# Kernel tuning notes

Measured on AMD Instinct MI355X. Metric: run time of the kernel, lower is better.

Reference implementation:

```python
import jax, jax.numpy as jnp
import numpy as np

QUALITY = 95
X_MIN, X_MAX = 0.0, 1.0

# JPEG Annex K base quantization tables
_LUMA = np.array([
    [16, 11, 10, 16, 24, 40, 51, 61],
    [12, 12, 14, 19, 26, 58, 60, 55],
    [14, 13, 16, 24, 40, 57, 69, 56],
    [14, 17, 22, 29, 51, 87, 80, 62],
    [18, 22, 37, 56, 68, 109, 103, 77],
    [24, 35, 55, 64, 81, 104, 113, 92],
    [49, 64, 78, 87, 103, 121, 120, 101],
    [72, 92, 95, 98, 112, 100, 103, 99]], dtype=np.float32)
_CHROMA = np.array([
    [17, 18, 24, 47, 99, 99, 99, 99],
    [18, 21, 26, 66, 99, 99, 99, 99],
    [24, 26, 56, 99, 99, 99, 99, 99],
    [47, 66, 99, 99, 99, 99, 99, 99],
    [99, 99, 99, 99, 99, 99, 99, 99],
    [99, 99, 99, 99, 99, 99, 99, 99],
    [99, 99, 99, 99, 99, 99, 99, 99],
    [99, 99, 99, 99, 99, 99, 99, 99]], dtype=np.float32)

def _qtable(base, quality):
    # libjpeg quality scaling (quality >= 50 branch)
    scale = 5000.0 / quality if quality < 50 else 200.0 - 2.0 * quality
    return np.clip(np.floor((base * scale + 50.0) / 100.0), 1.0, 255.0).astype(np.float32)

_QL = jnp.asarray(_qtable(_LUMA, QUALITY))
_QC = jnp.asarray(_qtable(_CHROMA, QUALITY))

# Orthonormal 8x8 DCT-II matrix
_k = np.arange(8)
_D = np.sqrt(2.0 / 8.0) * np.cos((2 * _k[None, :] + 1) * _k[:, None] * np.pi / 16.0)
_D[0, :] /= np.sqrt(2.0)
_D = jnp.asarray(_D.astype(np.float32))

def _jpeg_channel(ch, table):
    """8x8 block DCT -> quantize(round) -> dequantize -> IDCT. ch: [B,H,W] level-shifted."""
    B, H, W = ch.shape
    xb = ch.reshape(B, H // 8, 8, W // 8, 8)
    coef = jnp.einsum('ki,bhiwj,lj->bhkwl', _D, xb, _D)
    t = table[None, None, :, None, :]
    deq = jnp.round(coef / t) * t
    rec = jnp.einsum('ki,bhkwl,lj->bhiwj', _D, deq, _D)
    return rec.reshape(B, H, W)

def _jpeg_roundtrip(x255):
    """x255: [B,H,W,3] float values in [0,255]. Simulates JPEG encode+decode (4:2:0)."""
    r, g, b = x255[..., 0], x255[..., 1], x255[..., 2]
    # JFIF RGB -> YCbCr
    y = 0.299 * r + 0.587 * g + 0.114 * b
    cb = -0.168736 * r - 0.331264 * g + 0.5 * b + 128.0
    cr = 0.5 * r - 0.418688 * g - 0.081312 * b + 128.0
    # Luma at full resolution
    y2 = _jpeg_channel(y - 128.0, _QL) + 128.0
    # Chroma: 2x2 average downsample (4:2:0), codec, nearest upsample
    def down(c):
        B, H, W = c.shape
        return c.reshape(B, H // 2, 2, W // 2, 2).mean(axis=(2, 4))
    def up(c):
        return jnp.repeat(jnp.repeat(c, 2, axis=1), 2, axis=2)
    cb2 = up(_jpeg_channel(down(cb) - 128.0, _QC) + 128.0)
    cr2 = up(_jpeg_channel(down(cr) - 128.0, _QC) + 128.0)
    # YCbCr -> RGB
    r2 = y2 + 1.402 * (cr2 - 128.0)
    g2 = y2 - 0.344136 * (cb2 - 128.0) - 0.714136 * (cr2 - 128.0)
    b2 = y2 + 1.772 * (cb2 - 128.0)
    rgb = jnp.stack([r2, g2, b2], axis=-1)
    return jnp.round(jnp.clip(rgb, 0.0, 255.0))  # decoded uint8 values


def setup_inputs() -> dict:
    key = jax.random.key(0)
    x = jax.random.uniform(key, (32, 512, 512, 3), dtype=jnp.float32)
    return {"x": x}


def reference(x):
    # inputs -> uint8 pixel values (tf.cast truncation; values are >= 0)
    x255 = jnp.clip(jnp.floor((x - X_MIN) / ((X_MAX - X_MIN) / 255.0)), 0.0, 255.0)
    dec = _jpeg_roundtrip(x255)
    # back to input range/dtype
    return dec / (255.0 / (X_MAX - X_MIN)) + X_MIN
```

## Files before the change

### kernel.cpp

```cpp
#include <hip/hip_runtime.h>
#include <cstddef>

static constexpr float D8[8][8] = {
  { 0.35355339059327373f, 0.35355339059327373f, 0.35355339059327373f, 0.35355339059327373f,
    0.35355339059327373f, 0.35355339059327373f, 0.35355339059327373f, 0.35355339059327373f},
  { 0.4903926402016152f,  0.4157348061512726f,  0.27778511650980114f, 0.09754516100806417f,
   -0.09754516100806417f,-0.27778511650980114f,-0.4157348061512726f, -0.4903926402016152f},
  { 0.46193976625564337f, 0.19134171618254492f,-0.19134171618254492f,-0.46193976625564337f,
   -0.46193976625564337f,-0.19134171618254492f, 0.19134171618254492f, 0.46193976625564337f},
  { 0.4157348061512726f, -0.09754516100806417f,-0.4903926402016152f, -0.27778511650980114f,
    0.27778511650980114f, 0.4903926402016152f,  0.09754516100806417f,-0.4157348061512726f},
  { 0.35355339059327373f,-0.35355339059327373f,-0.35355339059327373f, 0.35355339059327373f,
    0.35355339059327373f,-0.35355339059327373f,-0.35355339059327373f, 0.35355339059327373f},
  { 0.27778511650980114f,-0.4903926402016152f,  0.09754516100806417f, 0.4157348061512726f,
   -0.4157348061512726f, -0.09754516100806417f, 0.4903926402016152f, -0.27778511650980114f},
  { 0.19134171618254492f,-0.46193976625564337f, 0.46193976625564337f,-0.19134171618254492f,
   -0.19134171618254492f, 0.46193976625564337f,-0.46193976625564337f, 0.19134171618254492f},
  { 0.09754516100806417f,-0.27778511650980114f, 0.4157348061512726f, -0.4903926402016152f,
    0.4903926402016152f, -0.4157348061512726f,  0.27778511650980114f,-0.09754516100806417f},
};

static constexpr float QLt[8][8] = {
  {2,1,1,2,2,4,5,6},
  {1,1,1,2,3,6,6,6},
  {1,1,2,2,4,6,7,6},
  {1,2,2,3,5,9,8,6},
  {2,2,4,6,7,11,10,8},
  {2,4,6,6,8,10,11,9},
  {5,6,8,9,10,12,12,10},
  {7,9,10,10,11,10,10,10},
};
static constexpr float QCt[8][8] = {
  {2,2,2,5,10,10,10,10},
  {2,2,3,7,10,10,10,10},
  {2,3,6,10,10,10,10,10},
  {5,7,10,10,10,10,10,10},
  {10,10,10,10,10,10,10,10},
  {10,10,10,10,10,10,10,10},
  {10,10,10,10,10,10,10,10},
  {10,10,10,10,10,10,10,10},
};

static constexpr float C255  = (float)(1.0/255.0);
static constexpr float RC255 = 1.0f / C255;

__device__ __forceinline__ float exact_div(float x, float c, float r) {
  float q0 = x * r;
  float e  = fmaf(-c, q0, x);
  return fmaf(e, r, q0);
}

__device__ __forceinline__ void dct8(const float x[8], float u[8]) {
  #pragma unroll
  for (int k = 0; k < 8; ++k) {
    float a = D8[k][0] * x[0];
    #pragma unroll
    for (int j = 1; j < 8; ++j) a += D8[k][j] * x[j];
    u[k] = a;
  }
}

__device__ __forceinline__ void idct8(const float x[8], float u[8]) {
  #pragma unroll
  for (int j = 0; j < 8; ++j) {
    float a = x[0] * D8[0][j];
    #pragma unroll
    for (int m = 1; m < 8; ++m) a += x[m] * D8[m][j];
    u[j] = a;
  }
}

__device__ __forceinline__ void xpose_scr(float v[8], int l, float* S) {
  #pragma unroll
  for (int m = 0; m < 8; ++m) S[m*13 + l] = v[m];
  asm volatile("" ::: "memory");
  float u[8];
  #pragma unroll
  for (int m = 0; m < 8; ++m) u[m] = S[l*13 + m];
  asm volatile("" ::: "memory");
  #pragma unroll
  for (int m = 0; m < 8; ++m) v[m] = u[m];
}

__device__ __forceinline__ void quant8(float v[8], const float* QT, const float* RQ) {
  float4 Q0 = *(const float4*)&QT[0];
  float4 Q1 = *(const float4*)&QT[4];
  float4 R0 = *(const float4*)&RQ[0];
  float4 R1 = *(const float4*)&RQ[4];
  float qv[8] = {Q0.x,Q0.y,Q0.z,Q0.w,Q1.x,Q1.y,Q1.z,Q1.w};
  float rv[8] = {R0.x,R0.y,R0.z,R0.w,R1.x,R1.y,R1.z,R1.w};
  #pragma unroll
  for (int m = 0; m < 8; ++m)
    v[m] = rintf(exact_div(v[m], qv[m], rv[m])) * qv[m];
}

__device__ __forceinline__ void jblk8(float v[8], int l, float* S,
                                      const float* QT, const float* RQ) {
  float u[8];
  dct8(v, u);
  xpose_scr(u, l, S);
  dct8(u, v);
  quant8(v, QT, RQ);
  idct8(v, u);
  xpose_scr(u, l, S);
  idct8(u, v);
}

__global__ __launch_bounds__(256) void jpeg_rt(const float* __restrict__ in,
                                               float* __restrict__ out)
{
  __shared__ __align__(16) float Yp[16][132];
  __shared__ __align__(16) float Scr[32][104];
  __shared__ __align__(16) float Cbp[8][68];
  __shared__ __align__(16) float Crp[8][68];
  __shared__ __align__(16) float QTs[2][8][8];
  __shared__ __align__(16) float RQs[2][8][8];

  const int t   = threadIdx.x;
  const int tx  = blockIdx.x;
  const int ty  = blockIdx.y;
  const int img = blockIdx.z;

  const int pr = t >> 5;
  const int pc = t & 31;

  if (t < 128) {
    const int pl = t >> 6, i = (t >> 3) & 7, m = t & 7;
    const float q = pl ? QCt[m][i] : QLt[m][i];
    QTs[pl][i][m] = q;
    RQs[pl][i][m] = 1.0f / q;
  }

  {
    float yv[2][4];
    float cbv[2][4], crv[2][4];
    #pragma unroll
    for (int rr = 0; rr < 2; ++rr) {
      const size_t grow = (size_t)img * 512 + (size_t)(ty*16 + 2*pr + rr);
      const float* rp = in + (grow*512 + (size_t)(tx*128 + 4*pc))*3;
      float4 A = ((const float4*)rp)[0];
      float4 Bq = ((const float4*)rp)[1];
      float4 Cq = ((const float4*)rp)[2];
      float px[12] = {A.x,A.y,A.z,A.w,Bq.x,Bq.y,Bq.z,Bq.w,Cq.x,Cq.y,Cq.z,Cq.w};
      #pragma unroll
      for (int p = 0; p < 4; ++p) {
        float r = floorf(exact_div(px[3*p+0], C255, RC255));
        float g = floorf(exact_div(px[3*p+1], C255, RC255));
        float b = floorf(exact_div(px[3*p+2], C255, RC255));
        float y  =  0.299f*r + 0.587f*g + 0.114f*b;
        float cb = -0.168736f*r - 0.331264f*g + 0.5f*b + 128.0f;
        float cr =  0.5f*r - 0.418688f*g - 0.081312f*b + 128.0f;
        yv[rr][p]  = y - 128.0f;
        cbv[rr][p] = cb;
        crv[rr][p] = cr;
      }
    }
    *(float4*)&Yp[2*pr+0][4*pc] = make_float4(yv[0][0],yv[0][1],yv[0][2],yv[0][3]);
    *(float4*)&Yp[2*pr+1][4*pc] = make_float4(yv[1][0],yv[1][1],yv[1][2],yv[1][3]);
    float cb0 = ((cbv[0][0]+cbv[0][1]) + (cbv[1][0]+cbv[1][1]))*0.25f - 128.0f;
    float cb1 = ((cbv[0][2]+cbv[0][3]) + (cbv[1][2]+cbv[1][3]))*0.25f - 128.0f;
    float cr0 = ((crv[0][0]+crv[0][1]) + (crv[1][0]+crv[1][1]))*0.25f - 128.0f;
    float cr1 = ((crv[0][2]+crv[0][3]) + (crv[1][2]+crv[1][3]))*0.25f - 128.0f;
    *(float2*)&Cbp[pr][2*pc] = make_float2(cb0, cb1);
    *(float2*)&Crp[pr][2*pc] = make_float2(cr0, cr1);
  }
  __syncthreads();

  {
    const int b = t >> 3, l = t & 7;
    const int br = b >> 4, bc = b & 15;
    float* rowp = &Yp[br*8 + l][bc*8];
    float4 L0 = *(const float4*)&rowp[0];
    float4 L1 = *(const float4*)&rowp[4];
    float v[8] = {L0.x, L0.y, L0.z, L0.w, L1.x, L1.y, L1.z, L1.w};
    jblk8(v, l, &Scr[b][0], &QTs[0][l][0], &RQs[0][l][0]);
    *(float4*)&rowp[0] = make_float4(v[0],v[1],v[2],v[3]);
    *(float4*)&rowp[4] = make_float4(v[4],v[5],v[6],v[7]);
  }
  if (t < 128) {
    const int g = t >> 3, l = t & 7;
    float* plane = (g & 8) ? &Crp[0][0] : &Cbp[0][0];
    float* rowp = plane + l*68 + (g & 7)*8;
    float4 L0 = *(const float4*)&rowp[0];
    float4 L1 = *(const float4*)&rowp[4];
    float v[8] = {L0.x, L0.y, L0.z, L0.w, L1.x, L1.y, L1.z, L1.w};
    jblk8(v, l, &Scr[g][0], &QTs[1][l][0], &RQs[1][l][0]);
    *(float4*)&rowp[0] = make_float4(v[0],v[1],v[2],v[3]);
    *(float4*)&rowp[4] = make_float4(v[4],v[5],v[6],v[7]);
  }
  __syncthreads();

  {
    float4 Y0 = *(const float4*)&Yp[2*pr+0][4*pc];
    float4 Y1 = *(const float4*)&Yp[2*pr+1][4*pc];
    float y0[4] = {Y0.x, Y0.y, Y0.z, Y0.w};
    float y1[4] = {Y1.x, Y1.y, Y1.z, Y1.w};
    float2 cbp2 = *(const float2*)&Cbp[pr][2*pc];
    float2 crp2 = *(const float2*)&Crp[pr][2*pc];
    float cbq[2] = {cbp2.x, cbp2.y};
    float crq[2] = {crp2.x, crp2.y};
    #pragma unroll
    for (int rr = 0; rr < 2; ++rr) {
      float ov[12];
      #pragma unroll
      for (int p = 0; p < 4; ++p) {
        float y2  = (rr ? y1[p] : y0[p]) + 128.0f;
        float cb2 = cbq[p>>1] + 128.0f;
        float cr2 = crq[p>>1] + 128.0f;
        float r2 = y2 + 1.402f*(cr2 - 128.0f);
        float g2 = y2 - 0.344136f*(cb2 - 128.0f) - 0.714136f*(cr2 - 128.0f);
        float b2 = y2 + 1.772f*(cb2 - 128.0f);
        ov[3*p+0] = rintf(fminf(fmaxf(r2, 0.0f), 255.0f)) * C255;
        ov[3*p+1] = rintf(fminf(fmaxf(g2, 0.0f), 255.0f)) * C255;
        ov[3*p+2] = rintf(fminf(fmaxf(b2, 0.0f), 255.0f)) * C255;
      }
      const size_t grow = (size_t)img * 512 + (size_t)(ty*16 + 2*pr + rr);
      float* op = out + (grow*512 + (size_t)(tx*128 + 4*pc))*3;
      ((float4*)op)[0] = make_float4(ov[0],ov[1],ov[2],ov[3]);
      ((float4*)op)[1] = make_float4(ov[4],ov[5],ov[6],ov[7]);
      ((float4*)op)[2] = make_float4(ov[8],ov[9],ov[10],ov[11]);
    }
  }
}

extern "C" void kernel_launch(void* const* d_in, const int* in_sizes, int n_in,
                              void* d_out, int out_size, void* d_ws, size_t ws_size,
                              hipStream_t stream) {
  (void)in_sizes; (void)n_in; (void)d_ws; (void)ws_size; (void)out_size;
  const float* x = (const float*)d_in[0];
  float* out = (float*)d_out;
  dim3 grid(4, 32, 32);
  jpeg_rt<<<grid, dim3(256), 0, stream>>>(x, out);
}
```

Measured before the change: 179.7 us.

## Split fused JPEG kernel into chroma pass and luma+reconstruct pass via workspace

Splits the single fused kernel into two launches. The first computes downsampled chroma and its DCT round trip into a workspace buffer. The second recomputes luma per block, runs its DCT, reads the chroma from the workspace and writes RGB. This removes the shared-memory staging and the work imbalance of the fused kernel. In exchange the input is read twice, there is an extra 16 MB workspace round trip, and a second launch. The old fused kernel is kept as a fallback when no workspace is available.

```diff
diff --git a/kernel.cpp b/kernel.cpp
--- a/kernel.cpp
+++ b/kernel.cpp
@@ -106,8 +106,152 @@
   idct8(u, v);
 }
 
-__global__ __launch_bounds__(256) void jpeg_rt(const float* __restrict__ in,
+__global__ __launch_bounds__(256) void chroma_k(const float* __restrict__ in,
+                                                float* __restrict__ ws)
+{
+  __shared__ __align__(16) float Scr[32][104];
+  __shared__ __align__(16) float QTc[8][8];
+  __shared__ __align__(16) float RQc[8][8];
+
+  const int t   = threadIdx.x;
+  const int g   = t >> 3;
+  const int l   = t & 7;
+  const int ry  = blockIdx.x;
+  const int img = blockIdx.y;
+
+  if (t < 64) {
+    const int i = t >> 3, m = t & 7;
+    const float q = QCt[m][i];
+    QTc[i][m] = q;
+    RQc[i][m] = 1.0f / q;
+  }
+
+  float scb[8], scr[8];
+  #pragma unroll
+  for (int rr = 0; rr < 2; ++rr) {
+    const int row = ry*16 + 2*l + rr;
+    const float* bp = in + ((size_t)img*512 + row)*1536 + (size_t)g*48;
+    #pragma unroll
+    for (int cq = 0; cq < 4; ++cq) {
+      float4 A = ((const float4*)bp)[cq*3+0];
+      float4 B = ((const float4*)bp)[cq*3+1];
+      float4 C = ((const float4*)bp)[cq*3+2];
+      float px[12] = {A.x,A.y,A.z,A.w,B.x,B.y,B.z,B.w,C.x,C.y,C.z,C.w};
+      float cbv[4], crv[4];
+      #pragma unroll
+      for (int p = 0; p < 4; ++p) {
+        float r = floorf(exact_div(px[3*p+0], C255, RC255));
+        float gg = floorf(exact_div(px[3*p+1], C255, RC255));
+        float b = floorf(exact_div(px[3*p+2], C255, RC255));
+        cbv[p] = -0.168736f*r - 0.331264f*gg + 0.5f*b + 128.0f;
+        crv[p] =  0.5f*r - 0.418688f*gg - 0.081312f*b + 128.0f;
+      }
+      const float hb0 = cbv[0]+cbv[1], hb1 = cbv[2]+cbv[3];
+      const float hr0 = crv[0]+crv[1], hr1 = crv[2]+crv[3];
+      if (rr == 0) { scb[2*cq] = hb0; scb[2*cq+1] = hb1;
+                     scr[2*cq] = hr0; scr[2*cq+1] = hr1; }
+      else         { scb[2*cq] += hb0; scb[2*cq+1] += hb1;
+                     scr[2*cq] += hr0; scr[2*cq+1] += hr1; }
+    }
+  }
+  float vcb[8], vcr[8];
+  #pragma unroll
+  for (int k = 0; k < 8; ++k) {
+    vcb[k] = scb[k]*0.25f - 128.0f;
+    vcr[k] = scr[k]*0.25f - 128.0f;
+  }
+  __syncthreads();
+
+  jblk8(vcb, l, &Scr[g][0], &QTc[l][0], &RQc[l][0]);
+  jblk8(vcr, l, &Scr[g][0], &QTc[l][0], &RQc[l][0]);
+
+  float* wp = ws + (size_t)img*131072 + (size_t)(ry*8 + l)*256 + g*8;
+  *(float4*)&wp[0]       = make_float4(vcb[0],vcb[1],vcb[2],vcb[3]);
+  *(float4*)&wp[4]       = make_float4(vcb[4],vcb[5],vcb[6],vcb[7]);
+  *(float4*)&wp[65536]   = make_float4(vcr[0],vcr[1],vcr[2],vcr[3]);
+  *(float4*)&wp[65540]   = make_float4(vcr[4],vcr[5],vcr[6],vcr[7]);
+}
+
+__global__ __launch_bounds__(256) void recon_k(const float* __restrict__ in,
+                                               const float* __restrict__ ws,
                                                float* __restrict__ out)
+{
+  __shared__ __align__(16) float Scr[32][104];
+  __shared__ __align__(16) float QTl[8][8];
+  __shared__ __align__(16) float RQl[8][8];
+
+  const int t   = threadIdx.x;
+  const int g   = t >> 3;
+  const int l   = t & 7;
+  const int br  = g >> 4;
+  const int bc  = g & 15;
+  const int tx  = blockIdx.x;
+  const int ty  = blockIdx.y;
+  const int img = blockIdx.z;
+
+  if (t < 64) {
+    const int i = t >> 3, m = t & 7;
+    const float q = QLt[m][i];
+    QTl[i][m] = q;
+    RQl[i][m] = 1.0f / q;
+  }
+
+  const int row  = ty*16 + br*8 + l;
+  const int col0 = tx*128 + bc*8;
+  const float* rp = in + ((size_t)img*512 + row)*1536 + (size_t)col0*3;
+  float4 P0 = ((const float4*)rp)[0];
+  float4 P1 = ((const float4*)rp)[1];
+  float4 P2 = ((const float4*)rp)[2];
+  float4 P3 = ((const float4*)rp)[3];
+  float4 P4 = ((const float4*)rp)[4];
+  float4 P5 = ((const float4*)rp)[5];
+  float px[24] = {P0.x,P0.y,P0.z,P0.w,P1.x,P1.y,P1.z,P1.w,
+                  P2.x,P2.y,P2.z,P2.w,P3.x,P3.y,P3.z,P3.w,
+                  P4.x,P4.y,P4.z,P4.w,P5.x,P5.y,P5.z,P5.w};
+  float vY[8];
+  #pragma unroll
+  for (int p = 0; p < 8; ++p) {
+    float r = floorf(exact_div(px[3*p+0], C255, RC255));
+    float gg = floorf(exact_div(px[3*p+1], C255, RC255));
+    float b = floorf(exact_div(px[3*p+2], C255, RC255));
+    vY[p] = (0.299f*r + 0.587f*gg + 0.114f*b) - 128.0f;
+  }
+  __syncthreads();
+
+  jblk8(vY, l, &Scr[g][0], &QTl[l][0], &RQl[l][0]);
+
+  const int crow = row >> 1;
+  const int ccol = tx*64 + bc*4;
+  const float* cp = ws + (size_t)img*131072 + (size_t)crow*256 + ccol;
+  float4 Cb4 = *(const float4*)cp;
+  float4 Cr4 = *(const float4*)(cp + 65536);
+  float cbq[4] = {Cb4.x, Cb4.y, Cb4.z, Cb4.w};
+  float crq[4] = {Cr4.x, Cr4.y, Cr4.z, Cr4.w};
+
+  float ov[24];
+  #pragma unroll
+  for (int p = 0; p < 8; ++p) {
+    float y2  = vY[p] + 128.0f;
+    float cb2 = cbq[p>>1] + 128.0f;
+    float cr2 = crq[p>>1] + 128.0f;
+    float r2 = y2 + 1.402f*(cr2 - 128.0f);
+    float g2 = y2 - 0.344136f*(cb2 - 128.0f) - 0.714136f*(cr2 - 128.0f);
+    float b2 = y2 + 1.772f*(cb2 - 128.0f);
+    ov[3*p+0] = rintf(fminf(fmaxf(r2, 0.0f), 255.0f)) * C255;
+    ov[3*p+1] = rintf(fminf(fmaxf(g2, 0.0f), 255.0f)) * C255;
+    ov[3*p+2] = rintf(fminf(fmaxf(b2, 0.0f), 255.0f)) * C255;
+  }
+  float* op = out + ((size_t)img*512 + row)*1536 + (size_t)col0*3;
+  ((float4*)op)[0] = make_float4(ov[0], ov[1], ov[2], ov[3]);
+  ((float4*)op)[1] = make_float4(ov[4], ov[5], ov[6], ov[7]);
+  ((float4*)op)[2] = make_float4(ov[8], ov[9], ov[10],ov[11]);
+  ((float4*)op)[3] = make_float4(ov[12],ov[13],ov[14],ov[15]);
+  ((float4*)op)[4] = make_float4(ov[16],ov[17],ov[18],ov[19]);
+  ((float4*)op)[5] = make_float4(ov[20],ov[21],ov[22],ov[23]);
+}
+
+__global__ __launch_bounds__(256) void jpeg_rt_fb(const float* __restrict__ in,
+                                                  float* __restrict__ out)
 {
   __shared__ __align__(16) float Yp[16][132];
   __shared__ __align__(16) float Scr[32][104];
@@ -120,7 +264,6 @@
   const int tx  = blockIdx.x;
   const int ty  = blockIdx.y;
   const int img = blockIdx.z;
-
   const int pr = t >> 5;
   const int pc = t & 31;
 
@@ -132,8 +275,7 @@
   }
 
   {
-    float yv[2][4];
-    float cbv[2][4], crv[2][4];
+    float yv[2][4], cbv[2][4], crv[2][4];
     #pragma unroll
     for (int rr = 0; rr < 2; ++rr) {
       const size_t grow = (size_t)img * 512 + (size_t)(ty*16 + 2*pr + rr);
@@ -226,9 +368,15 @@
 extern "C" void kernel_launch(void* const* d_in, const int* in_sizes, int n_in,
                               void* d_out, int out_size, void* d_ws, size_t ws_size,
                               hipStream_t stream) {
-  (void)in_sizes; (void)n_in; (void)d_ws; (void)ws_size; (void)out_size;
+  (void)in_sizes; (void)n_in; (void)out_size;
   const float* x = (const float*)d_in[0];
   float* out = (float*)d_out;
-  dim3 grid(4, 32, 32);
-  jpeg_rt<<<grid, dim3(256), 0, stream>>>(x, out);
-}
+  const size_t WS_NEED = (size_t)32 * 2 * 256 * 256 * 4;
+  if (d_ws != nullptr && ws_size >= WS_NEED) {
+    float* ws = (float*)d_ws;
+    chroma_k<<<dim3(32, 32, 1), dim3(256), 0, stream>>>(x, ws);
+    recon_k<<<dim3(4, 32, 32), dim3(256), 0, stream>>>(x, ws, out);
+  } else {
+    jpeg_rt_fb<<<dim3(4, 32, 32), dim3(256), 0, stream>>>(x, out);
+  }
+}
```

After: 209.2 us. 1.16x slower.
